# Performance work log

Hardware: AMD Instinct MI355X
Metric: run time of the kernel (lower is better)

Reference implementation:

```python
import jax, jax.numpy as jnp
import numpy as np

ALPHA = 0.2      # LeakyReLU negative slope
NEG_INF = -9e15  # mask value from the original code

def setup_inputs() -> dict:
    key = jax.random.key(0)
    k1, k2, k3, k4 = jax.random.split(key, 4)
    B, M, F_IN, F_OUT = 16, 2048, 128, 64
    h = jax.random.normal(k1, (B, M, F_IN), dtype=jnp.float32)
    adj = jax.random.randint(k2, (B, M, M), 0, 2, dtype=jnp.int32)
    W = jax.random.normal(k3, (F_IN, F_OUT), dtype=jnp.float32) * 0.1
    a = jax.random.normal(k4, (2 * F_OUT, 1), dtype=jnp.float32) * 0.1
    return {"h": h, "adj": adj, "W": W, "a": a}

def reference(h, adj, W, a):
    # h: [B,M,Fin], adj: [B,M,M], W: [Fin,E], a: [2E,1]
    Wh = jnp.matmul(h, W)                      # [B,M,E]
    E = Wh.shape[-1]
    a1, a2 = a[:E, 0], a[E:, 0]
    # decompose a^T [Wh_i || Wh_j] = (Wh_i . a1) + (Wh_j . a2)
    f1 = Wh @ a1                               # [B,M] (source/query term)
    f2 = Wh @ a2                               # [B,M] (target/key term)
    e = jax.nn.leaky_relu(f1[:, :, None] + f2[:, None, :], negative_slope=ALPHA)  # [B,M,M]
    scores = jnp.where(adj > 0, e, NEG_INF)
    attn = jax.nn.softmax(scores, axis=-1)     # [B,M,M]  (dropout p=0 / eval mode)
    h_prime = jnp.matmul(attn, Wh)             # [B,M,E]
    return jax.nn.elu(h_prime)                 # concat=True branch
```

## Files before the change

kernel.cpp:

```cpp
#include <hip/hip_runtime.h>


#define M_     2048
#define FIN_   128
#define F_     64
#define ALPHA_ 0.2f
#define ROWS_  32
#define TS_    36
#define WT_    132

typedef float  float4_ __attribute__((ext_vector_type(4)));
typedef short  short4_ __attribute__((ext_vector_type(4)));
typedef short  short8  __attribute__((ext_vector_type(8)));
typedef int    int4_   __attribute__((ext_vector_type(4)));
typedef unsigned int u32x4 __attribute__((ext_vector_type(4)));
typedef unsigned short u16;
typedef unsigned int   u32;

static __device__ __forceinline__ u32 cvtpk(float lo, float hi) {
    u32 r;
    asm("v_cvt_pk_bf16_f32 %0, %1, %2" : "=v"(r) : "v"(lo), "v"(hi));
    return r;
}

__global__ __launch_bounds__(256, 4) void k_gat4(
    const float* __restrict__ h, const int* __restrict__ adj,
    const float* __restrict__ W, const float* __restrict__ a,
    float* __restrict__ out)
{
    __shared__ float a_s[2 * F_];
    __shared__ float wa1[FIN_], wa2[FIN_];
    __shared__ float f1s[ROWS_];
    __shared__ float dens[ROWS_];
    __shared__ char  dyn[18688];

    u16*   hTbuf0 = (u16*)dyn;
    u16*   hTbuf1 = (u16*)(dyn + 9216);
    float* f2t0   = (float*)(dyn + 18432);
    float* f2t1   = (float*)(dyn + 18560);
    float* Tsum   = (float*)dyn;

    const int tid  = threadIdx.x;
    const int w    = tid >> 6;
    const int l    = tid & 63;
    const int lc   = l & 15;
    const int quad = l >> 4;

    const u32 bid = blockIdx.x;
    const u32 lg  = (bid & 7) * 128 + (bid >> 3);
    const int b   = lg >> 6;
    const int i0  = (lg & 63) * ROWS_;

    const int rg = w & 1;
    const int nh = w >> 1;
    const int fo = tid & 15;
    const int tp = tid >> 4;

    if (tid < 128) a_s[tid] = a[tid];
    __syncthreads();

    if (tid < FIN_) {
        float s1 = 0.f, s2 = 0.f;
#pragma unroll 8
        for (int n = 0; n < F_; ++n) {
            float wv = W[tid * F_ + n];
            s1 += wv * a_s[n];
            s2 += wv * a_s[F_ + n];
        }
        wa1[tid] = s1;
        wa2[tid] = s2;
    }
    __syncthreads();

    {
        const int r = tid >> 3, k0 = (tid & 7) * 16;
        const float* hp = h + ((size_t)(b * M_ + i0 + r)) * FIN_ + k0;
        float s = 0.f;
#pragma unroll
        for (int k = 0; k < 16; ++k) s += hp[k] * wa1[k0 + k];
        s += __shfl_xor(s, 1, 64);
        s += __shfl_xor(s, 2, 64);
        s += __shfl_xor(s, 4, 64);
        if ((tid & 7) == 0) f1s[r] = s;
    }

    float4_ w2a = *(const float4_*)(wa2 + fo * 8);
    float4_ w2b = *(const float4_*)(wa2 + fo * 8 + 4);

    const int*   aprow  = adj + ((size_t)(b * M_ + i0 + rg * 16 + lc)) * M_ + quad * 8;
    const float* hstage = h + ((size_t)(b * M_ + 2 * tp)) * FIN_ + fo * 8;

    int4_   aA0 = *(const int4_*)(aprow);
    int4_   aA1 = *(const int4_*)(aprow + 4);
    int4_   aB0 = *(const int4_*)(aprow + 32);
    int4_   aB1 = *(const int4_*)(aprow + 36);
    int4_   aC0 = *(const int4_*)(aprow + 64);
    int4_   aC1 = *(const int4_*)(aprow + 68);
    float4_ hE0 = *(const float4_*)(hstage);
    float4_ hE1 = *(const float4_*)(hstage + 4);
    float4_ hO0 = *(const float4_*)(hstage + FIN_);
    float4_ hO1 = *(const float4_*)(hstage + FIN_ + 4);

    __syncthreads();

    const float f1r = f1s[rg * 16 + lc];
    float denacc = 0.f;
    float4_ acc0 = {0.f,0.f,0.f,0.f}, acc1 = {0.f,0.f,0.f,0.f};
    float4_ acc2 = {0.f,0.f,0.f,0.f}, acc3 = {0.f,0.f,0.f,0.f};

#pragma unroll 2
    for (int t = 0; t < 64; ++t) {
        u16*   hT  = (t & 1) ? hTbuf1 : hTbuf0;
        float* f2c = (t & 1) ? f2t1   : f2t0;
        const int jn = (t < 63 ? t + 1 : 63) * 32;
        const int jp = (t < 61 ? t + 3 : 63) * 32;

        int4_   nA0 = *(const int4_*)(aprow + jp);
        int4_   nA1 = *(const int4_*)(aprow + jp + 4);
        float4_ nE0 = *(const float4_*)(hstage + (size_t)jn * FIN_);
        float4_ nE1 = *(const float4_*)(hstage + (size_t)jn * FIN_ + 4);
        float4_ nO0 = *(const float4_*)(hstage + (size_t)jn * FIN_ + FIN_);
        float4_ nO1 = *(const float4_*)(hstage + (size_t)jn * FIN_ + FIN_ + 4);

        {
            u16* wbase = hT + fo * (8 * TS_) + 2 * (tp ^ (fo & 12));
            float fp0 = 0.f, fp1 = 0.f;
#pragma unroll
            for (int kk = 0; kk < 8; ++kk) {
                float ev = (kk < 4) ? hE0[kk] : hE1[kk - 4];
                float od = (kk < 4) ? hO0[kk] : hO1[kk - 4];
                *(u32*)(wbase + kk * TS_) = cvtpk(ev, od);
                float wk = (kk < 4) ? w2a[kk] : w2b[kk - 4];
                fp0 += ev * wk;
                fp1 += od * wk;
            }
            fp0 += __shfl_xor(fp0, 1, 64); fp1 += __shfl_xor(fp1, 1, 64);
            fp0 += __shfl_xor(fp0, 2, 64); fp1 += __shfl_xor(fp1, 2, 64);
            fp0 += __shfl_xor(fp0, 4, 64); fp1 += __shfl_xor(fp1, 4, 64);
            fp0 += __shfl_xor(fp0, 8, 64); fp1 += __shfl_xor(fp1, 8, 64);
            if (fo == 0) { f2c[2 * tp] = fp0; f2c[2 * tp + 1] = fp1; }
        }

        asm volatile("s_waitcnt lgkmcnt(0)" ::: "memory");
        __builtin_amdgcn_s_barrier();
        __builtin_amdgcn_sched_barrier(0);

        float4_ g0 = *(const float4_*)(f2c + quad * 8);
        float4_ g1 = *(const float4_*)(f2c + quad * 8 + 4);
        u32x4 pw;
        float d = 0.f;
#define SC(GE, GO, AE, AO, IDX)                                 \
        {                                                       \
            float xe = f1r + (GE); xe = fmaxf(xe, ALPHA_ * xe); \
            float xo = f1r + (GO); xo = fmaxf(xo, ALPHA_ * xo); \
            float ee = ((AE) > 0) ? __expf(xe) : 0.f;           \
            float eo = ((AO) > 0) ? __expf(xo) : 0.f;           \
            u32 pk = cvtpk(ee, eo);                             \
            d += __uint_as_float(pk << 16);                     \
            d += __uint_as_float(pk & 0xFFFF0000u);             \
            pw[IDX] = pk;                                       \
        }
        SC(g0[0], g0[1], aA0[0], aA0[1], 0)
        SC(g0[2], g0[3], aA0[2], aA0[3], 1)
        SC(g1[0], g1[1], aA1[0], aA1[1], 2)
        SC(g1[2], g1[3], aA1[2], aA1[3], 3)
#undef SC
        denacc += d;
        short8 af = __builtin_bit_cast(short8, pw);

#define MT(C, ACC)                                                             \
        {                                                                      \
            const u16* bp = hT + ((nh * 4 + (C)) * 16 + lc) * TS_              \
                          + (((quad * 4) ^ (((nh * 4 + (C)) * 2) & 12)) << 1); \
            short4_ b0 = *(const short4_*)bp;                                  \
            short4_ b1 = *(const short4_*)(bp + 4);                            \
            short8 bf;                                                         \
            bf[0] = b0[0]; bf[1] = b0[1]; bf[2] = b0[2]; bf[3] = b0[3];        \
            bf[4] = b1[0]; bf[5] = b1[1]; bf[6] = b1[2]; bf[7] = b1[3];        \
            ACC = __builtin_amdgcn_mfma_f32_16x16x32_bf16(af, bf, ACC, 0, 0, 0); \
        }
        MT(0, acc0) MT(1, acc1) MT(2, acc2) MT(3, acc3)
#undef MT

        aA0 = aB0; aA1 = aB1; aB0 = aC0; aB1 = aC1; aC0 = nA0; aC1 = nA1;
        hE0 = nE0; hE1 = nE1; hO0 = nO0; hO1 = nO1;
    }

    denacc += __shfl_xor(denacc, 16, 64);
    denacc += __shfl_xor(denacc, 32, 64);
    if (nh == 0 && quad == 0) dens[rg * 16 + lc] = denacc;
    __syncthreads();

#pragma unroll
    for (int mm = 0; mm < 4; ++mm) {
        float* tr = Tsum + (rg * 16 + quad * 4 + mm) * WT_ + nh * 64 + lc;
        tr[0]  = acc0[mm];
        tr[16] = acc1[mm];
        tr[32] = acc2[mm];
        tr[48] = acc3[mm];
    }
    __syncthreads();

    {
        const int r  = tid >> 3;
        const int n0 = (tid & 7) * 8;
        const float den  = dens[r];
        const float rden = (den > 0.f) ? (1.f / den) : 0.f;
        float u[8];
#pragma unroll
        for (int nn = 0; nn < 8; ++nn) u[nn] = 0.f;
#pragma unroll 4
        for (int k = 0; k < FIN_; ++k) {
            const float tv = Tsum[r * WT_ + k];
            float4_ wv0 = *(const float4_*)(W + k * F_ + n0);
            float4_ wv1 = *(const float4_*)(W + k * F_ + n0 + 4);
            u[0] += tv * wv0[0]; u[1] += tv * wv0[1];
            u[2] += tv * wv0[2]; u[3] += tv * wv0[3];
            u[4] += tv * wv1[0]; u[5] += tv * wv1[1];
            u[6] += tv * wv1[2]; u[7] += tv * wv1[3];
        }
        float4_ o0, o1;
#pragma unroll
        for (int nn = 0; nn < 8; ++nn) {
            float hp = u[nn] * rden;
            float o  = hp > 0.f ? hp : expm1f(hp);
            if (nn < 4) o0[nn] = o; else o1[nn - 4] = o;
        }
        float* op = out + ((size_t)(b * M_ + i0 + r)) * F_ + n0;
        *(float4_*)op       = o0;
        *(float4_*)(op + 4) = o1;
    }
}

extern "C" void kernel_launch(void* const* d_in, const int* in_sizes, int n_in,
                              void* d_out, int out_size, void* d_ws, size_t ws_size,
                              hipStream_t stream)
{
    (void)out_size; (void)d_ws; (void)ws_size;
    const float* h  = (const float*)d_in[0];
    const int* adjp = (const int*)d_in[1];
    const float* Wp = (const float*)d_in[2];
    const float* ap = (const float*)d_in[3];
    for (int i = 0; i < n_in; ++i) {
        long s = in_sizes[i];
        if      (s == 4194304L)  h    = (const float*)d_in[i];
        else if (s == 67108864L) adjp = (const int*)d_in[i];
        else if (s == 8192L)     Wp   = (const float*)d_in[i];
        else if (s == 128L)      ap   = (const float*)d_in[i];
    }
    k_gat4<<<1024, 256, 0, stream>>>(h, adjp, Wp, ap, (float*)d_out);
}
```

Before: 483.5 us.

## Split into prep kernel writing bf16 MFMA-layout h and f1/f2, then main kernel

A new prep kernel converts h to bf16 once, stored pre-swizzled in MFMA B-operand layout in the workspace, and computes f1/f2 for all rows. The main kernel then loads B fragments straight from global into registers. This removes the per-tile LDS transpose, the f2 recomputation and the per-iteration barrier. Each block now covers 64 rows with 8 MFMA accumulators per wave and half as many blocks, so every block no longer re-reads and re-converts the full fp32 h. The costs are a second launch, higher register pressure (launch bounds 2) and reliance on an 8MB+ workspace.

Measured after the change: 428.0 us. 1.13x faster.

```diff
diff --git a/kernel.cpp b/kernel.cpp
--- a/kernel.cpp
+++ b/kernel.cpp
@@ -5,12 +5,10 @@
 #define FIN_   128
 #define F_     64
 #define ALPHA_ 0.2f
-#define ROWS_  32
-#define TS_    36
+#define HS_    132
 #define WT_    132
 
 typedef float  float4_ __attribute__((ext_vector_type(4)));
-typedef short  short4_ __attribute__((ext_vector_type(4)));
 typedef short  short8  __attribute__((ext_vector_type(8)));
 typedef int    int4_   __attribute__((ext_vector_type(4)));
 typedef unsigned int u32x4 __attribute__((ext_vector_type(4)));
@@ -23,40 +21,29 @@
     return r;
 }
 
-__global__ __launch_bounds__(256, 4) void k_gat4(
-    const float* __restrict__ h, const int* __restrict__ adj,
-    const float* __restrict__ W, const float* __restrict__ a,
-    float* __restrict__ out)
+__global__ __launch_bounds__(256, 4) void k_prep(
+    const float* __restrict__ h, const float* __restrict__ W,
+    const float* __restrict__ a, u16* __restrict__ hbf,
+    float* __restrict__ f1all, float* __restrict__ f2all)
 {
     __shared__ float a_s[2 * F_];
     __shared__ float wa1[FIN_], wa2[FIN_];
-    __shared__ float f1s[ROWS_];
-    __shared__ float dens[ROWS_];
-    __shared__ char  dyn[18688];
-
-    u16*   hTbuf0 = (u16*)dyn;
-    u16*   hTbuf1 = (u16*)(dyn + 9216);
-    float* f2t0   = (float*)(dyn + 18432);
-    float* f2t1   = (float*)(dyn + 18560);
-    float* Tsum   = (float*)dyn;
-
-    const int tid  = threadIdx.x;
-    const int w    = tid >> 6;
-    const int l    = tid & 63;
-    const int lc   = l & 15;
-    const int quad = l >> 4;
-
+    __shared__ float hs[32 * HS_];
+
+    const int tid = threadIdx.x;
     const u32 bid = blockIdx.x;
     const u32 lg  = (bid & 7) * 128 + (bid >> 3);
     const int b   = lg >> 6;
-    const int i0  = (lg & 63) * ROWS_;
-
-    const int rg = w & 1;
-    const int nh = w >> 1;
-    const int fo = tid & 15;
-    const int tp = tid >> 4;
+    const int t   = lg & 63;
 
     if (tid < 128) a_s[tid] = a[tid];
+
+    const int tok = tid >> 3, f0 = (tid & 7) * 16;
+    const float* hp = h + ((size_t)(b * M_ + t * 32 + tok)) * FIN_ + f0;
+    float4_ x0 = *(const float4_*)hp;
+    float4_ x1 = *(const float4_*)(hp + 4);
+    float4_ x2 = *(const float4_*)(hp + 8);
+    float4_ x3 = *(const float4_*)(hp + 12);
     __syncthreads();
 
     if (tid < FIN_) {
@@ -70,83 +57,116 @@
         wa1[tid] = s1;
         wa2[tid] = s2;
     }
-    __syncthreads();
+
+    float* hr = hs + tok * HS_ + f0;
+    *(float4_*)(hr)      = x0;
+    *(float4_*)(hr + 4)  = x1;
+    *(float4_*)(hr + 8)  = x2;
+    *(float4_*)(hr + 12) = x3;
+    __syncthreads();
+
+    {
+        const int l = tid & 63, lc = l & 15, q = l >> 4;
+        const int nt0 = (tid >> 6) * 2;
+        u32x4* ob = (u32x4*)hbf + ((size_t)(b * 64 + t)) * 8 * 64;
+#pragma unroll
+        for (int ni = 0; ni < 2; ++ni) {
+            const int nt = nt0 + ni;
+            const float* cp = hs + (q * 8) * HS_ + nt * 16 + lc;
+            u32x4 wv;
+            wv[0] = cvtpk(cp[0 * HS_], cp[1 * HS_]);
+            wv[1] = cvtpk(cp[2 * HS_], cp[3 * HS_]);
+            wv[2] = cvtpk(cp[4 * HS_], cp[5 * HS_]);
+            wv[3] = cvtpk(cp[6 * HS_], cp[7 * HS_]);
+            ob[nt * 64 + l] = wv;
+        }
+    }
 
     {
         const int r = tid >> 3, k0 = (tid & 7) * 16;
-        const float* hp = h + ((size_t)(b * M_ + i0 + r)) * FIN_ + k0;
-        float s = 0.f;
-#pragma unroll
-        for (int k = 0; k < 16; ++k) s += hp[k] * wa1[k0 + k];
-        s += __shfl_xor(s, 1, 64);
-        s += __shfl_xor(s, 2, 64);
-        s += __shfl_xor(s, 4, 64);
-        if ((tid & 7) == 0) f1s[r] = s;
-    }
-
-    float4_ w2a = *(const float4_*)(wa2 + fo * 8);
-    float4_ w2b = *(const float4_*)(wa2 + fo * 8 + 4);
-
-    const int*   aprow  = adj + ((size_t)(b * M_ + i0 + rg * 16 + lc)) * M_ + quad * 8;
-    const float* hstage = h + ((size_t)(b * M_ + 2 * tp)) * FIN_ + fo * 8;
-
-    int4_   aA0 = *(const int4_*)(aprow);
-    int4_   aA1 = *(const int4_*)(aprow + 4);
-    int4_   aB0 = *(const int4_*)(aprow + 32);
-    int4_   aB1 = *(const int4_*)(aprow + 36);
-    int4_   aC0 = *(const int4_*)(aprow + 64);
-    int4_   aC1 = *(const int4_*)(aprow + 68);
-    float4_ hE0 = *(const float4_*)(hstage);
-    float4_ hE1 = *(const float4_*)(hstage + 4);
-    float4_ hO0 = *(const float4_*)(hstage + FIN_);
-    float4_ hO1 = *(const float4_*)(hstage + FIN_ + 4);
-
-    __syncthreads();
-
-    const float f1r = f1s[rg * 16 + lc];
+        const float* rp = hs + r * HS_ + k0;
+        float s1 = 0.f, s2 = 0.f;
+#pragma unroll
+        for (int k = 0; k < 16; ++k) {
+            s1 += rp[k] * wa1[k0 + k];
+            s2 += rp[k] * wa2[k0 + k];
+        }
+        s1 += __shfl_xor(s1, 1, 64); s2 += __shfl_xor(s2, 1, 64);
+        s1 += __shfl_xor(s1, 2, 64); s2 += __shfl_xor(s2, 2, 64);
+        s1 += __shfl_xor(s1, 4, 64); s2 += __shfl_xor(s2, 4, 64);
+        if ((tid & 7) == 0) {
+            f1all[b * M_ + t * 32 + r] = s1;
+            f2all[b * M_ + t * 32 + r] = s2;
+        }
+    }
+}
+
+__global__ __launch_bounds__(256, 2) void k_main(
+    const int* __restrict__ adj, const u16* __restrict__ hbf,
+    const float* __restrict__ f1all, const float* __restrict__ f2all,
+    const float* __restrict__ W, float* __restrict__ out)
+{
+    __shared__ char  dyn[WT_ * 64 * 4];
+    __shared__ float dens[64];
+
+    float* f2s  = (float*)dyn;
+    float* Tsum = (float*)dyn;
+
+    const int tid  = threadIdx.x;
+    const int w    = tid >> 6;
+    const int l    = tid & 63;
+    const int lc   = l & 15;
+    const int quad = l >> 4;
+
+    const u32 bid = blockIdx.x;
+    const u32 lg  = (bid & 7) * 64 + (bid >> 3);
+    const int b   = lg >> 5;
+    const int i0  = (lg & 31) * 64;
+    const int rowbase = i0 + w * 16;
+
+    {
+        const int o = tid * 8;
+        float4_ v0 = *(const float4_*)(f2all + b * M_ + o);
+        float4_ v1 = *(const float4_*)(f2all + b * M_ + o + 4);
+        *(float4_*)(f2s + o)     = v0;
+        *(float4_*)(f2s + o + 4) = v1;
+    }
+
+    const float f1r = f1all[b * M_ + rowbase + lc];
+    const int* aprow = adj + ((size_t)(b * M_ + rowbase + lc)) * M_ + quad * 8;
+    const u32x4* hb  = (const u32x4*)hbf + ((size_t)b * 64) * 8 * 64 + l;
+
+    int4_ aA0 = *(const int4_*)(aprow);
+    int4_ aA1 = *(const int4_*)(aprow + 4);
+    int4_ aB0 = *(const int4_*)(aprow + 32);
+    int4_ aB1 = *(const int4_*)(aprow + 36);
+    int4_ aC0 = *(const int4_*)(aprow + 64);
+    int4_ aC1 = *(const int4_*)(aprow + 68);
+    u32x4 bC[8];
+#pragma unroll
+    for (int nt = 0; nt < 8; ++nt) bC[nt] = hb[nt * 64];
+
+    __syncthreads();
+
     float denacc = 0.f;
-    float4_ acc0 = {0.f,0.f,0.f,0.f}, acc1 = {0.f,0.f,0.f,0.f};
-    float4_ acc2 = {0.f,0.f,0.f,0.f}, acc3 = {0.f,0.f,0.f,0.f};
+    float4_ acc[8];
+#pragma unroll
+    for (int nt = 0; nt < 8; ++nt) acc[nt] = (float4_){0.f, 0.f, 0.f, 0.f};
 
 #pragma unroll 2
     for (int t = 0; t < 64; ++t) {
-        u16*   hT  = (t & 1) ? hTbuf1 : hTbuf0;
-        float* f2c = (t & 1) ? f2t1   : f2t0;
-        const int jn = (t < 63 ? t + 1 : 63) * 32;
         const int jp = (t < 61 ? t + 3 : 63) * 32;
-
-        int4_   nA0 = *(const int4_*)(aprow + jp);
-        int4_   nA1 = *(const int4_*)(aprow + jp + 4);
-        float4_ nE0 = *(const float4_*)(hstage + (size_t)jn * FIN_);
-        float4_ nE1 = *(const float4_*)(hstage + (size_t)jn * FIN_ + 4);
-        float4_ nO0 = *(const float4_*)(hstage + (size_t)jn * FIN_ + FIN_);
-        float4_ nO1 = *(const float4_*)(hstage + (size_t)jn * FIN_ + FIN_ + 4);
-
-        {
-            u16* wbase = hT + fo * (8 * TS_) + 2 * (tp ^ (fo & 12));
-            float fp0 = 0.f, fp1 = 0.f;
-#pragma unroll
-            for (int kk = 0; kk < 8; ++kk) {
-                float ev = (kk < 4) ? hE0[kk] : hE1[kk - 4];
-                float od = (kk < 4) ? hO0[kk] : hO1[kk - 4];
-                *(u32*)(wbase + kk * TS_) = cvtpk(ev, od);
-                float wk = (kk < 4) ? w2a[kk] : w2b[kk - 4];
-                fp0 += ev * wk;
-                fp1 += od * wk;
-            }
-            fp0 += __shfl_xor(fp0, 1, 64); fp1 += __shfl_xor(fp1, 1, 64);
-            fp0 += __shfl_xor(fp0, 2, 64); fp1 += __shfl_xor(fp1, 2, 64);
-            fp0 += __shfl_xor(fp0, 4, 64); fp1 += __shfl_xor(fp1, 4, 64);
-            fp0 += __shfl_xor(fp0, 8, 64); fp1 += __shfl_xor(fp1, 8, 64);
-            if (fo == 0) { f2c[2 * tp] = fp0; f2c[2 * tp + 1] = fp1; }
-        }
-
-        asm volatile("s_waitcnt lgkmcnt(0)" ::: "memory");
-        __builtin_amdgcn_s_barrier();
-        __builtin_amdgcn_sched_barrier(0);
-
-        float4_ g0 = *(const float4_*)(f2c + quad * 8);
-        float4_ g1 = *(const float4_*)(f2c + quad * 8 + 4);
+        const int tn = (t < 63 ? t + 1 : 63);
+
+        int4_ nA0 = *(const int4_*)(aprow + jp);
+        int4_ nA1 = *(const int4_*)(aprow + jp + 4);
+        u32x4 bN[8];
+#pragma unroll
+        for (int nt = 0; nt < 8; ++nt) bN[nt] = hb[(tn * 8 + nt) * 64];
+
+        float4_ g0 = *(const float4_*)(f2s + t * 32 + quad * 8);
+        float4_ g1 = *(const float4_*)(f2s + t * 32 + quad * 8 + 4);
+
         u32x4 pw;
         float d = 0.f;
 #define SC(GE, GO, AE, AO, IDX)                                 \
@@ -166,43 +186,33 @@
         SC(g1[2], g1[3], aA1[2], aA1[3], 3)
 #undef SC
         denacc += d;
-        short8 af = __builtin_bit_cast(short8, pw);
-
-#define MT(C, ACC)                                                             \
-        {                                                                      \
-            const u16* bp = hT + ((nh * 4 + (C)) * 16 + lc) * TS_              \
-                          + (((quad * 4) ^ (((nh * 4 + (C)) * 2) & 12)) << 1); \
-            short4_ b0 = *(const short4_*)bp;                                  \
-            short4_ b1 = *(const short4_*)(bp + 4);                            \
-            short8 bf;                                                         \
-            bf[0] = b0[0]; bf[1] = b0[1]; bf[2] = b0[2]; bf[3] = b0[3];        \
-            bf[4] = b1[0]; bf[5] = b1[1]; bf[6] = b1[2]; bf[7] = b1[3];        \
-            ACC = __builtin_amdgcn_mfma_f32_16x16x32_bf16(af, bf, ACC, 0, 0, 0); \
-        }
-        MT(0, acc0) MT(1, acc1) MT(2, acc2) MT(3, acc3)
-#undef MT
+        const short8 af = __builtin_bit_cast(short8, pw);
+
+#pragma unroll
+        for (int nt = 0; nt < 8; ++nt)
+            acc[nt] = __builtin_amdgcn_mfma_f32_16x16x32_bf16(
+                af, __builtin_bit_cast(short8, bC[nt]), acc[nt], 0, 0, 0);
 
         aA0 = aB0; aA1 = aB1; aB0 = aC0; aB1 = aC1; aC0 = nA0; aC1 = nA1;
-        hE0 = nE0; hE1 = nE1; hO0 = nO0; hO1 = nO1;
+#pragma unroll
+        for (int nt = 0; nt < 8; ++nt) bC[nt] = bN[nt];
     }
 
     denacc += __shfl_xor(denacc, 16, 64);
     denacc += __shfl_xor(denacc, 32, 64);
-    if (nh == 0 && quad == 0) dens[rg * 16 + lc] = denacc;
-    __syncthreads();
-
-#pragma unroll
-    for (int mm = 0; mm < 4; ++mm) {
-        float* tr = Tsum + (rg * 16 + quad * 4 + mm) * WT_ + nh * 64 + lc;
-        tr[0]  = acc0[mm];
-        tr[16] = acc1[mm];
-        tr[32] = acc2[mm];
-        tr[48] = acc3[mm];
-    }
-    __syncthreads();
-
-    {
-        const int r  = tid >> 3;
+    if (quad == 0) dens[w * 16 + lc] = denacc;
+    __syncthreads();
+
+#pragma unroll
+    for (int nt = 0; nt < 8; ++nt)
+#pragma unroll
+        for (int mm = 0; mm < 4; ++mm)
+            Tsum[(w * 16 + quad * 4 + mm) * WT_ + nt * 16 + lc] = acc[nt][mm];
+    __syncthreads();
+
+#pragma unroll
+    for (int rr = 0; rr < 2; ++rr) {
+        const int r  = (tid >> 3) + rr * 32;
         const int n0 = (tid & 7) * 8;
         const float den  = dens[r];
         const float rden = (den > 0.f) ? (1.f / den) : 0.f;
@@ -236,7 +246,7 @@
                               void* d_out, int out_size, void* d_ws, size_t ws_size,
                               hipStream_t stream)
 {
-    (void)out_size; (void)d_ws; (void)ws_size;
+    (void)out_size; (void)ws_size;
     const float* h  = (const float*)d_in[0];
     const int* adjp = (const int*)d_in[1];
     const float* Wp = (const float*)d_in[2];
@@ -248,5 +258,9 @@
         else if (s == 8192L)     Wp   = (const float*)d_in[i];
         else if (s == 128L)      ap   = (const float*)d_in[i];
     }
-    k_gat4<<<1024, 256, 0, stream>>>(h, adjp, Wp, ap, (float*)d_out);
-}
+    u16*   hbf   = (u16*)d_ws;
+    float* f1all = (float*)((char*)d_ws + (8u << 20));
+    float* f2all = f1all + 16 * M_;
+    k_prep<<<1024, 256, 0, stream>>>(h, Wp, ap, hbf, f1all, f2all);
+    k_main<<<512, 256, 0, stream>>>(adjp, hbf, f1all, f2all, Wp, (float*)d_out);
+}
```
